# Kernel tuning notes

Hardware: AMD Instinct MI355X
Metric: run time of the kernel (lower is better)

Reference implementation:

```python
import jax, jax.numpy as jnp
import numpy as np

SOGLIA = 0.333
# db4 analysis lowpass filter stored time-reversed (= rec_lo scaling filter), matching
# pytorch_wavelets prep_filt_afb1d (weight = dec_lo[::-1]) used with cross-correlation.
DB4_H = np.array([0.23037781330885523, 0.7148465705525415, 0.6308807679295904,
                  -0.02798376941698385, -0.18703481171888114, 0.030841381835986965,
                  0.032883011666982945, -0.010597401784997278], dtype=np.float32)


def dwt_lo(x):
    # Single-level DWT lowpass with mode='zero' (pytorch_wavelets afb1d semantics).
    # x: (B, N, D), filtering + stride-2 downsample along token axis N.
    B, N, D = x.shape
    L = DB4_H.shape[0]
    outsize = (N + L - 1) // 2            # pywt.dwt_coeff_len for zero mode
    p = 2 * (outsize - 1) - N + L         # total pad needed
    if p % 2 == 1:                        # odd: extra zero at the end first
        x = jnp.pad(x, ((0, 0), (0, 1), (0, 0)))
    x = jnp.pad(x, ((0, 0), (p // 2, p // 2), (0, 0)))
    k = jnp.tile(jnp.asarray(DB4_H, x.dtype)[None, None, :], (D, 1, 1))  # (D,1,L) depthwise
    y = jax.lax.conv_general_dilated(x.transpose(0, 2, 1), k, window_strides=(2,),
                                     padding='VALID', feature_group_count=D)
    return y.transpose(0, 2, 1)           # (B, outsize, D)


def compute_gini(probs):
    B, N = probs.shape
    sp = jnp.sort(probs, axis=1)
    idx = jnp.arange(1, N + 1, dtype=sp.dtype)
    return 2.0 * (idx * sp).sum(axis=1) / (N * sp.sum(axis=1) + 1e-8) - (N + 1) / N


def setup_inputs() -> dict:
    key = jax.random.key(0)
    k1, k2 = jax.random.split(key)
    x = jax.random.normal(k1, (256, 197, 768), dtype=jnp.float32)
    cls_attention_map = jax.random.uniform(k2, (256, 196), dtype=jnp.float32)
    return {"x": x, "cls_attention_map": cls_attention_map}


def reference(x, cls_attention_map):
    B, N, D = x.shape
    cls_tok, patch = x[:, :1], x[:, 1:]            # (B,1,D), (B,N-1,D)
    gini = compute_gini(cls_attention_map)
    level2 = gini > SOGLIA                         # route: True -> J=2, False -> J=1
    y1 = dwt_lo(patch)                             # level-1 lowpass (B, len1, D)
    y2 = dwt_lo(y1)                                # level-2 lowpass (B, len2, D)
    len1, len2 = y1.shape[1], y2.shape[1]
    y2p = jnp.pad(y2, ((0, 0), (0, len1 - len2), (0, 0)))
    final_patches = jnp.where(level2[:, None, None], y2p, y1)   # dense-expert combine
    out_len = jnp.where(level2, len2, len1)
    final_x = jnp.concatenate([cls_tok, final_patches], axis=1)  # (B, len1+1, D)
    mask = jnp.arange(len1)[None, :] < out_len[:, None]
    mask = jnp.concatenate([jnp.ones((B, 1), dtype=bool), mask], axis=1)
    return final_x, mask
```

## Files before the change

### kernel.cpp

```cpp
#include <hip/hip_runtime.h>

#define NB   256
#define NTOK 197
#define NP   196
#define ND   768
#define LEN1 101
#define LEN2 54
#define OUTROWS 102
#define NWG (NB * OUTROWS)

typedef float f4 __attribute__((ext_vector_type(4)));

__global__ __launch_bounds__(256)
void gini_kernel(const float* __restrict__ attn, int* __restrict__ flags) {
    __shared__ float  row[NP];
    __shared__ double sS[256];
    __shared__ double sT[256];
    const int b   = blockIdx.x;
    const int tid = threadIdx.x;
    if (tid < NP) row[tid] = attn[b * NP + tid];
    __syncthreads();
    double sj = 0.0, tj = 0.0;
    if (tid < NP) {
        const float p = row[tid];
        int rank = 1;
        for (int k = 0; k < NP; ++k) {
            const float q = row[k];
            rank += (q < p) || (q == p && k < tid);
        }
        sj = (double)rank * (double)p;
        tj = (double)p;
    }
    sS[tid] = sj; sT[tid] = tj;
    __syncthreads();
    for (int off = 128; off > 0; off >>= 1) {
        if (tid < off) { sS[tid] += sS[tid + off]; sT[tid] += sT[tid + off]; }
        __syncthreads();
    }
    if (tid == 0) {
        const double S = sS[0], T = sT[0];
        const double gini = 2.0 * S / ((double)NP * T + 1e-8)
                          - (double)(NP + 1) / (double)NP;
        flags[b] = (gini > (double)0.333f) ? 1 : 0;
    }
}

__global__ __launch_bounds__(192)
void dwt_kernel(const float* __restrict__ x, const int* __restrict__ flags,
                float* __restrict__ out_x, float* __restrict__ out_mask) {
    const float h[8] = {0.23037781330885523f,  0.7148465705525415f,
                        0.6308807679295904f,  -0.02798376941698385f,
                       -0.18703481171888114f,  0.030841381835986965f,
                        0.032883011666982945f,-0.010597401784997278f};
    float g[22];
    #pragma unroll
    for (int m = 0; m < 22; ++m) {
        float s = 0.f;
        #pragma unroll
        for (int j = 0; j < 8; ++j) {
            const int l = m - 2 * j;
            if (0 <= l && l < 8) s += h[j] * h[l];
        }
        g[m] = s;
    }

    const int hw  = blockIdx.x;
    const int per = NWG / 8;
    const int bid = (hw & 7) * per + (hw >> 3);
    const int b = bid / OUTROWS;
    const int r = bid - b * OUTROWS;
    const int c = threadIdx.x;
    const int d0 = c * 4;

    const float* __restrict__ px = x + ((size_t)b * NTOK + 1) * ND + d0;
    float* __restrict__ po = out_x + ((size_t)b * OUTROWS + r) * ND + d0;
    const int flag = flags[b];

    if (r == 0) {
        const f4 cls = *(const f4*)(x + (size_t)b * NTOK * ND + d0);
        __builtin_nontemporal_store(cls, (f4*)po);
        if (c < OUTROWS) {
            const int outlen = flag ? LEN2 : LEN1;
            out_mask[b * OUTROWS + c] = (c == 0 || (c - 1) < outlen) ? 1.0f : 0.0f;
        }
        return;
    }

    const int t = r - 1;
    f4 y = {0.f, 0.f, 0.f, 0.f};
    if (!flag) {
        const int base = 2 * t - 6;
        #pragma unroll
        for (int l = 0; l < 8; ++l) {
            const int i = base + l;
            if (i >= 0 && i < NP) {
                const f4 v = *(const f4*)(px + (size_t)i * ND);
                y += h[l] * v;
            }
        }
    } else if (t < LEN2) {
        const int base = 4 * t - 18;
        #pragma unroll
        for (int m = 0; m < 22; ++m) {
            const int i = base + m;
            if (i >= 0 && i < NP) {
                const f4 v = *(const f4*)(px + (size_t)i * ND);
                y += g[m] * v;
            }
        }
    }
    __builtin_nontemporal_store(y, (f4*)po);
}

extern "C" void kernel_launch(void* const* d_in, const int* in_sizes, int n_in,
                              void* d_out, int out_size, void* d_ws, size_t ws_size,
                              hipStream_t stream) {
    const float* x    = (const float*)d_in[0];
    const float* attn = (const float*)d_in[1];
    float* out_x    = (float*)d_out;
    float* out_mask = (float*)d_out + (size_t)NB * OUTROWS * ND;
    int* flags = (int*)d_ws;

    gini_kernel<<<NB, 256, 0, stream>>>(attn, flags);
    dwt_kernel<<<NWG, 192, 0, stream>>>(x, flags, out_x, out_mask);
}
```

Before: 51.60 us.

## Compute eight output rows per workgroup and use wave-shuffle reduction in gini

The DWT kernel now assigns each workgroup a block of eight output rows per batch, not one row. Each loaded input row is reused across all overlapping filter taps in registers, which cuts redundant global/L2 loads and the workgroup count. Interior blocks skip bounds checks. The gini kernel vectorises its rank loop with float4 LDS reads and replaces the shared-memory tree reduction with wave shuffles, leaving one barrier. The cost is higher register pressure and fewer workgroups, which may reduce occupancy and latency hiding.

```diff
diff --git a/kernel.cpp b/kernel.cpp
--- a/kernel.cpp
+++ b/kernel.cpp
@@ -7,15 +7,16 @@
 #define LEN1 101
 #define LEN2 54
 #define OUTROWS 102
-#define NWG (NB * OUTROWS)
+#define QROWS 8
+#define NQ   13
+#define NWG  (NB * NQ)
 
 typedef float f4 __attribute__((ext_vector_type(4)));
 
 __global__ __launch_bounds__(256)
 void gini_kernel(const float* __restrict__ attn, int* __restrict__ flags) {
-    __shared__ float  row[NP];
-    __shared__ double sS[256];
-    __shared__ double sT[256];
+    __shared__ __align__(16) float row[NP];
+    __shared__ double wS[4], wT[4];
     const int b   = blockIdx.x;
     const int tid = threadIdx.x;
     if (tid < NP) row[tid] = attn[b * NP + tid];
@@ -24,21 +25,30 @@
     if (tid < NP) {
         const float p = row[tid];
         int rank = 1;
-        for (int k = 0; k < NP; ++k) {
-            const float q = row[k];
-            rank += (q < p) || (q == p && k < tid);
+        #pragma unroll 7
+        for (int k4 = 0; k4 < NP / 4; ++k4) {
+            const f4 qv = *(const f4*)&row[4 * k4];
+            #pragma unroll
+            for (int e = 0; e < 4; ++e) {
+                const float qe = qv[e];
+                const int idx = 4 * k4 + e;
+                rank += (qe < p) || (qe == p && idx < tid);
+            }
         }
         sj = (double)rank * (double)p;
         tj = (double)p;
     }
-    sS[tid] = sj; sT[tid] = tj;
+    #pragma unroll
+    for (int off = 32; off > 0; off >>= 1) {
+        sj += __shfl_down(sj, off);
+        tj += __shfl_down(tj, off);
+    }
+    const int wid = tid >> 6, lane = tid & 63;
+    if (lane == 0) { wS[wid] = sj; wT[wid] = tj; }
     __syncthreads();
-    for (int off = 128; off > 0; off >>= 1) {
-        if (tid < off) { sS[tid] += sS[tid + off]; sT[tid] += sT[tid + off]; }
-        __syncthreads();
-    }
     if (tid == 0) {
-        const double S = sS[0], T = sT[0];
+        const double S = wS[0] + wS[1] + wS[2] + wS[3];
+        const double T = wT[0] + wT[1] + wT[2] + wT[3];
         const double gini = 2.0 * S / ((double)NP * T + 1e-8)
                           - (double)(NP + 1) / (double)NP;
         flags[b] = (gini > (double)0.333f) ? 1 : 0;
@@ -52,7 +62,7 @@
                         0.6308807679295904f,  -0.02798376941698385f,
                        -0.18703481171888114f,  0.030841381835986965f,
                         0.032883011666982945f,-0.010597401784997278f};
-    float g[22];
+    float g2[22];
     #pragma unroll
     for (int m = 0; m < 22; ++m) {
         float s = 0.f;
@@ -61,55 +71,75 @@
             const int l = m - 2 * j;
             if (0 <= l && l < 8) s += h[j] * h[l];
         }
-        g[m] = s;
+        g2[m] = s;
     }
 
     const int hw  = blockIdx.x;
     const int per = NWG / 8;
     const int bid = (hw & 7) * per + (hw >> 3);
-    const int b = bid / OUTROWS;
-    const int r = bid - b * OUTROWS;
-    const int c = threadIdx.x;
-    const int d0 = c * 4;
+    const int b   = bid / NQ;
+    const int q   = bid - b * NQ;
+    const int c   = threadIdx.x;
+    const int d0  = c * 4;
 
     const float* __restrict__ px = x + ((size_t)b * NTOK + 1) * ND + d0;
-    float* __restrict__ po = out_x + ((size_t)b * OUTROWS + r) * ND + d0;
-    const int flag = flags[b];
+    float* __restrict__ po = out_x + (size_t)b * OUTROWS * ND + d0;
+    const int flag  = flags[b];
+    const int rbase = q * QROWS;
+    const int jmax  = (rbase + QROWS <= OUTROWS) ? QROWS : (OUTROWS - rbase);
 
-    if (r == 0) {
-        const f4 cls = *(const f4*)(x + (size_t)b * NTOK * ND + d0);
-        __builtin_nontemporal_store(cls, (f4*)po);
+    f4 acc[QROWS];
+    #pragma unroll
+    for (int j = 0; j < QROWS; ++j) acc[j] = (f4){0.f, 0.f, 0.f, 0.f};
+
+    auto raw = [&](int i) -> f4 { return *(const f4*)(px + (size_t)i * ND); };
+    auto clamped = [&](int i) -> f4 {
+        return (i >= 0 && i < NP) ? *(const f4*)(px + (size_t)i * ND)
+                                  : (f4){0.f, 0.f, 0.f, 0.f};
+    };
+
+    if (!flag) {
+        const int lo = 16 * q - 8;
+        auto run = [&](auto ld) {
+            #pragma unroll
+            for (int k = 0; k < 22; ++k) {
+                const f4 v = ld(lo + k);
+                #pragma unroll
+                for (int j = 0; j < QROWS; ++j) {
+                    const int l = k - 2 * j;
+                    if (0 <= l && l < 8) acc[j] += h[l] * v;
+                }
+            }
+        };
+        if (q >= 1 && q <= 11) run(raw); else run(clamped);
+    } else if (q <= 6) {
+        const int lo = 32 * q - 22;
+        auto run = [&](auto ld) {
+            #pragma unroll
+            for (int k = 0; k < 50; ++k) {
+                const f4 v = ld(lo + k);
+                #pragma unroll
+                for (int j = 0; j < QROWS; ++j) {
+                    const int m = k - 4 * j;
+                    if (0 <= m && m < 22) acc[j] += g2[m] * v;
+                }
+            }
+        };
+        if (q >= 1 && q <= 5) run(raw); else run(clamped);
+    }
+
+    if (q == 0) {
+        acc[0] = *(const f4*)(x + (size_t)b * NTOK * ND + d0);
         if (c < OUTROWS) {
             const int outlen = flag ? LEN2 : LEN1;
             out_mask[b * OUTROWS + c] = (c == 0 || (c - 1) < outlen) ? 1.0f : 0.0f;
         }
-        return;
     }
 
-    const int t = r - 1;
-    f4 y = {0.f, 0.f, 0.f, 0.f};
-    if (!flag) {
-        const int base = 2 * t - 6;
-        #pragma unroll
-        for (int l = 0; l < 8; ++l) {
-            const int i = base + l;
-            if (i >= 0 && i < NP) {
-                const f4 v = *(const f4*)(px + (size_t)i * ND);
-                y += h[l] * v;
-            }
-        }
-    } else if (t < LEN2) {
-        const int base = 4 * t - 18;
-        #pragma unroll
-        for (int m = 0; m < 22; ++m) {
-            const int i = base + m;
-            if (i >= 0 && i < NP) {
-                const f4 v = *(const f4*)(px + (size_t)i * ND);
-                y += g[m] * v;
-            }
-        }
-    }
-    __builtin_nontemporal_store(y, (f4*)po);
+    #pragma unroll
+    for (int j = 0; j < QROWS; ++j)
+        if (j < jmax)
+            __builtin_nontemporal_store(acc[j], (f4*)(po + (size_t)(rbase + j) * ND));
 }
 
 extern "C" void kernel_launch(void* const* d_in, const int* in_sizes, int n_in,
```

Result: faster. 46.68 us (-9.5%).
